# Optimization experiments

Hardware: AMD Instinct MI355X
Metric: run time of the kernel (lower is better)

Reference implementation:

```python
import jax, jax.numpy as jnp
import numpy as np

B, C, H, W = 8, 16, 64, 64
D, N = 1, 512  # embedding_dim, num_embeddings


def setup_inputs() -> dict:
    key = jax.random.key(0)
    k1, k2 = jax.random.split(key)
    x = jax.random.normal(k1, (B, C, H, W), dtype=jnp.float32)
    weight = jax.random.uniform(k2, (D, N), dtype=jnp.float32)  # torch.rand init
    return {"x": x, "weight": weight}


def reference(x, weight):
    b, c, h, w = x.shape
    # dist: [B,C,H,W,N] via broadcast (D==1), argmin over codebook axis
    dist = (x[..., None] - weight) ** 2
    argmin = jnp.argmin(dist, axis=-1)  # [B,C,H,W] int
    # faithful replication of index_select + view([B,H,W,C]) + permute(0,3,1,2)
    codes = jnp.take(weight.T, argmin.reshape(-1), axis=0)  # [B*C*H*W, 1]
    quantized = codes.reshape(b, h, w, c).transpose(0, 3, 1, 2)  # [B,C,H,W]
    e_latent_loss = jnp.mean((x - jax.lax.stop_gradient(quantized)) ** 2)
    q_latent_loss = jnp.mean((quantized - jax.lax.stop_gradient(x)) ** 2)
    # straight-through estimator
    quantized_st = x + jax.lax.stop_gradient(quantized - x)
    return quantized_st, q_latent_loss, e_latent_loss
```

## Files before the change

kernel.cpp:

```cpp
#include <hip/hip_runtime.h>
#include <hip/hip_bf16.h>


#define E_TOTAL 524288
#define NCODE   512
#define BLOCK   256
#define NBLOCKS (E_TOTAL / BLOCK)

__global__ __launch_bounds__(64) void vq_prep_kernel(
    const float* __restrict__ wt, float* __restrict__ sorted) {
  __shared__ float4 lw4[NCODE / 4];
  const int t = threadIdx.x;
  lw4[t] = ((const float4*)wt)[t];
  lw4[t + 64] = ((const float4*)wt)[t + 64];
  __syncthreads();

  const int i = blockIdx.x * 64 + t;
  const float v = ((const float*)lw4)[i];
  int r = 0;
#pragma unroll 8
  for (int j = 0; j < NCODE / 4; ++j) {
    const float4 u = lw4[j];
    const int n0 = 4 * j;
    r += (u.x < v || (u.x == v && (n0 + 0) < i)) ? 1 : 0;
    r += (u.y < v || (u.y == v && (n0 + 1) < i)) ? 1 : 0;
    r += (u.z < v || (u.z == v && (n0 + 2) < i)) ? 1 : 0;
    r += (u.w < v || (u.w == v && (n0 + 3) < i)) ? 1 : 0;
  }
  sorted[r] = v;
}

__global__ __launch_bounds__(BLOCK) void vq_main_kernel(
    const float* __restrict__ x, const float* __restrict__ sorted,
    float* __restrict__ out, double* __restrict__ partial) {
  __shared__ float ls[NCODE + 2];
  __shared__ double lsum[BLOCK / 64];

  const int t = threadIdx.x;
  for (int k = t; k < NCODE; k += BLOCK) ls[k + 1] = sorted[k];
  if (t == 0) { ls[0] = -3.0e38f; ls[NCODE + 1] = 3.0e38f; }
  __syncthreads();

  const int o = blockIdx.x * BLOCK + t;
  const int w = o & 63;
  const int h = (o >> 6) & 63;
  const int c = (o >> 12) & 15;
  const int b = o >> 16;
  const int ip = b * 65536 + h * 1024 + w * 16 + c;
  const float xv = x[ip];

  unsigned idx = 0;
#pragma unroll
  for (unsigned step = NCODE / 2; step; step >>= 1) {
    const float sv = ls[idx + step];
    idx = (sv <= xv) ? idx + step : idx;
  }
  const float left = ls[idx];
  const float right = ls[idx + 1];
  const float dl = xv - left;  const float d2l = dl * dl;
  const float dr = xv - right; const float d2r = dr * dr;
  const float wq = (d2l <= d2r) ? left : right;

  out[o] = wq;

  const float diff = x[o] - wq;
  double ds = (double)diff * (double)diff;

#pragma unroll
  for (int off = 32; off > 0; off >>= 1) ds += __shfl_down(ds, off, 64);
  const int lane = t & 63, wave = t >> 6;
  if (lane == 0) lsum[wave] = ds;
  __syncthreads();
  if (t == 0) {
    double s = 0.0;
#pragma unroll
    for (int i = 0; i < BLOCK / 64; ++i) s += lsum[i];
    partial[blockIdx.x] = s;
  }
}

__global__ __launch_bounds__(BLOCK) void vq_reduce_kernel(
    const double* __restrict__ partial, float* __restrict__ out) {
  __shared__ double lsum[BLOCK / 64];
  const int t = threadIdx.x;
  double s = 0.0;
  for (int k = t; k < NBLOCKS; k += BLOCK) s += partial[k];
#pragma unroll
  for (int off = 32; off > 0; off >>= 1) s += __shfl_down(s, off, 64);
  const int lane = t & 63, wave = t >> 6;
  if (lane == 0) lsum[wave] = s;
  __syncthreads();
  if (t == 0) {
    double tot = 0.0;
#pragma unroll
    for (int i = 0; i < BLOCK / 64; ++i) tot += lsum[i];
    const float m = (float)(tot / (double)E_TOTAL);
    out[E_TOTAL] = m;
    out[E_TOTAL + 1] = m;
  }
}

extern "C" void kernel_launch(void* const* d_in, const int* in_sizes, int n_in,
                              void* d_out, int out_size, void* d_ws, size_t ws_size,
                              hipStream_t stream) {
  const float* x = (const float*)d_in[0];
  const float* wt = (const float*)d_in[1];
  float* out = (float*)d_out;
  float* sorted = (float*)d_ws;
  double* partial = (double*)((char*)d_ws + 4096);

  vq_prep_kernel<<<8, 64, 0, stream>>>(wt, sorted);
  vq_main_kernel<<<NBLOCKS, BLOCK, 0, stream>>>(x, sorted, out, partial);
  vq_reduce_kernel<<<1, BLOCK, 0, stream>>>(partial, out);
}
```

Before: 79.71 us.

## Process two elements per thread with skewed LDS codebook and early loads

Each thread now quantizes two adjacent outputs, running two interleaved binary searches over the sorted codebook and writing the pair as a single float2 store. This halves the block count, so each codebook fill into LDS and each partial-sum slot covers twice the work. The LDS index is skewed by one slot every 32 entries to reduce bank conflicts during the data-dependent search. Global loads of x are issued before the barrier to hide their latency. The unused upper sentinel is dropped. The trade-off is fewer resident blocks and more registers per thread.

```diff
diff --git a/kernel.cpp b/kernel.cpp
--- a/kernel.cpp
+++ b/kernel.cpp
@@ -5,7 +5,10 @@
 #define E_TOTAL 524288
 #define NCODE   512
 #define BLOCK   256
-#define NBLOCKS (E_TOTAL / BLOCK)
+#define M       2
+#define NBLOCKS_M (E_TOTAL / (BLOCK * M))
+
+#define SKEW(a) ((a) + ((a) >> 5))
 
 __global__ __launch_bounds__(64) void vq_prep_kernel(
     const float* __restrict__ wt, float* __restrict__ sorted) {
@@ -33,38 +36,46 @@
 __global__ __launch_bounds__(BLOCK) void vq_main_kernel(
     const float* __restrict__ x, const float* __restrict__ sorted,
     float* __restrict__ out, double* __restrict__ partial) {
-  __shared__ float ls[NCODE + 2];
+  __shared__ float ls[SKEW(NCODE + 1) + 1];
   __shared__ double lsum[BLOCK / 64];
 
   const int t = threadIdx.x;
-  for (int k = t; k < NCODE; k += BLOCK) ls[k + 1] = sorted[k];
-  if (t == 0) { ls[0] = -3.0e38f; ls[NCODE + 1] = 3.0e38f; }
+  const int tid = blockIdx.x * BLOCK + t;
+  const int o0 = tid * M;
+  const int w = o0 & 63;
+  const int h = (o0 >> 6) & 63;
+  const int c = (o0 >> 12) & 15;
+  const int b = o0 >> 16;
+  const int ip0 = b * 65536 + h * 1024 + w * 16 + c;
+
+  const float g0 = x[ip0];
+  const float g1 = x[ip0 + 16];
+  const float2 xo = ((const float2*)x)[tid];
+
+  for (int k = t; k < NCODE; k += BLOCK) ls[SKEW(k + 1)] = sorted[k];
+  if (t == 0) ls[SKEW(0)] = -3.0e38f;
   __syncthreads();
 
-  const int o = blockIdx.x * BLOCK + t;
-  const int w = o & 63;
-  const int h = (o >> 6) & 63;
-  const int c = (o >> 12) & 15;
-  const int b = o >> 16;
-  const int ip = b * 65536 + h * 1024 + w * 16 + c;
-  const float xv = x[ip];
-
-  unsigned idx = 0;
+  unsigned i0 = 0, i1 = 0;
 #pragma unroll
   for (unsigned step = NCODE / 2; step; step >>= 1) {
-    const float sv = ls[idx + step];
-    idx = (sv <= xv) ? idx + step : idx;
+    const float s0 = ls[SKEW(i0 + step)];
+    const float s1 = ls[SKEW(i1 + step)];
+    i0 = (s0 <= g0) ? i0 + step : i0;
+    i1 = (s1 <= g1) ? i1 + step : i1;
   }
-  const float left = ls[idx];
-  const float right = ls[idx + 1];
-  const float dl = xv - left;  const float d2l = dl * dl;
-  const float dr = xv - right; const float d2r = dr * dr;
-  const float wq = (d2l <= d2r) ? left : right;
+  const float l0 = ls[SKEW(i0)], r0 = ls[SKEW(i0 + 1)];
+  const float l1 = ls[SKEW(i1)], r1 = ls[SKEW(i1 + 1)];
+  const float dl0 = g0 - l0, dr0 = g0 - r0;
+  const float dl1 = g1 - l1, dr1 = g1 - r1;
+  const float wq0 = (dl0 * dl0 <= dr0 * dr0) ? l0 : r0;
+  const float wq1 = (dl1 * dl1 <= dr1 * dr1) ? l1 : r1;
 
-  out[o] = wq;
+  ((float2*)out)[tid] = make_float2(wq0, wq1);
 
-  const float diff = x[o] - wq;
-  double ds = (double)diff * (double)diff;
+  const float d0 = xo.x - wq0;
+  const float d1 = xo.y - wq1;
+  double ds = (double)d0 * (double)d0 + (double)d1 * (double)d1;
 
 #pragma unroll
   for (int off = 32; off > 0; off >>= 1) ds += __shfl_down(ds, off, 64);
@@ -84,7 +95,7 @@
   __shared__ double lsum[BLOCK / 64];
   const int t = threadIdx.x;
   double s = 0.0;
-  for (int k = t; k < NBLOCKS; k += BLOCK) s += partial[k];
+  for (int k = t; k < NBLOCKS_M; k += BLOCK) s += partial[k];
 #pragma unroll
   for (int off = 32; off > 0; off >>= 1) s += __shfl_down(s, off, 64);
   const int lane = t & 63, wave = t >> 6;
@@ -110,6 +121,6 @@
   double* partial = (double*)((char*)d_ws + 4096);
 
   vq_prep_kernel<<<8, 64, 0, stream>>>(wt, sorted);
-  vq_main_kernel<<<NBLOCKS, BLOCK, 0, stream>>>(x, sorted, out, partial);
+  vq_main_kernel<<<NBLOCKS_M, BLOCK, 0, stream>>>(x, sorted, out, partial);
   vq_reduce_kernel<<<1, BLOCK, 0, stream>>>(partial, out);
 }
```

Result: no change. 78.37 us (median of 2 runs) (-1.7%).
